# Kernel optimization log

Measured on AMD Instinct MI355X. Metric: run time of the kernel, lower is better.

Reference implementation:

```python
import jax, jax.numpy as jnp
import numpy as np

EPS = 1e-5
N = 2097152


def _bn(x, gamma, beta):
    # training-mode BatchNorm1d: biased batch stats over the batch dim
    mean = jnp.mean(x, axis=0)
    var = jnp.var(x, axis=0)
    return (x - mean) * jax.lax.rsqrt(var + EPS) * gamma + beta


def _block(x, W1, g, b, W2, b2):
    # Linear(no bias) -> BN -> ReLU -> Linear(bias)
    h = jax.nn.relu(_bn(x @ W1, g, b))
    return h @ W2 + b2


def setup_inputs() -> dict:
    key = jax.random.key(0)
    ks = jax.random.split(key, 32)
    i = iter(range(32))
    rn = lambda shape, s=0.1: (jax.random.normal(ks[next(i)], shape, dtype=jnp.float32) * s)
    d = {
        "rotation": jax.random.normal(ks[next(i)], (N, 9), dtype=jnp.float32),
        "transition": jax.random.normal(ks[next(i)], (N, 3), dtype=jnp.float32),
        # key net: 3->32 (no bias), BN32, 32->64
        "kW1": rn((3, 32)), "kg": jnp.ones(32), "kb": jnp.zeros(32),
        "kW2": rn((32, 64)), "kb2": rn((64,)),
        # query net: 9->32 (no bias), BN32, 32->64
        "qW1": rn((9, 32)), "qg": jnp.ones(32), "qb": jnp.zeros(32),
        "qW2": rn((32, 64)), "qb2": rn((64,)),
        # value net: 3->32 (no bias), BN32, 32->64
        "vW1": rn((3, 32)), "vg": jnp.ones(32), "vb": jnp.zeros(32),
        "vW2": rn((32, 64)), "vb2": rn((64,)),
        # decoder: 64->32(nb), BN32, ReLU, 32->16(nb), BN16, ReLU, 16->1(b), sigmoid
        "dW1": rn((64, 32)), "dg1": jnp.ones(32), "db1": jnp.zeros(32),
        "dW2": rn((32, 16)), "dg2": jnp.ones(16), "db2": jnp.zeros(16),
        "dW3": rn((16, 1)), "db3": rn((1,)),
    }
    return d


def reference(rotation, transition,
              kW1, kg, kb, kW2, kb2,
              qW1, qg, qb, qW2, qb2,
              vW1, vg, vb, vW2, vb2,
              dW1, dg1, db1, dW2, dg2, db2, dW3, db3):
    k = _block(transition, kW1, kg, kb, kW2, kb2)   # [N, 64]
    q = _block(rotation, qW1, qg, qb, qW2, qb2)     # [N, 64]
    v = _block(transition, vW1, vg, vb, vW2, vb2)   # [N, 64]
    attn = jax.nn.softmax(k * q, axis=-1) * v        # [N, 64]
    h = jax.nn.relu(_bn(attn @ dW1, dg1, db1))       # [N, 32]
    h = jax.nn.relu(_bn(h @ dW2, dg2, db2))          # [N, 16]
    out = jax.nn.sigmoid(h @ dW3 + db3)              # [N, 1]
    return out
```

## Files before the change

kernel.cpp:

```cpp
#include <hip/hip_runtime.h>

#define EPS 1e-5f
#define L2E 1.442695041f

typedef __attribute__((ext_vector_type(8))) short short8;
typedef __attribute__((ext_vector_type(4))) float f32x4;
#define MFMA16(a,b,c) __builtin_amdgcn_mfma_f32_16x16x32_bf16(a,b,c,0,0,0)

typedef float __attribute__((may_alias)) fal;
typedef unsigned short __attribute__((may_alias)) sal;
typedef unsigned int __attribute__((may_alias)) u32al;
typedef uint4 __attribute__((may_alias)) u4al;
typedef f32x4 __attribute__((may_alias)) f4al;

union U8 { short8 s; uint4 u; };

__device__ __forceinline__ float wred(float v){
#pragma unroll
  for(int m=32;m>=1;m>>=1) v += __shfl_xor(v,m,64);
  return v;
}

__device__ __forceinline__ unsigned short f2bf(float f){
  union{unsigned int i; float x;}v; v.x=f;
  unsigned int u=v.i;
  unsigned int r=(u + 0x7fffu + ((u>>16)&1u))>>16;
  return (unsigned short)r;
}
__device__ __forceinline__ unsigned cvtpk(float lo, float hi){
  unsigned r; asm("v_cvt_pk_bf16_f32 %0, %1, %2" : "=v"(r) : "v"(lo), "v"(hi)); return r;
}
__device__ __forceinline__ float bflo(unsigned int u){
  union{unsigned int i; float x;}v; v.i=u<<16; return v.x;
}
__device__ __forceinline__ float bfhi(unsigned int u){
  union{unsigned int i; float x;}v; v.i=u&0xffff0000u; return v.x;
}

__device__ __host__ __forceinline__ int kperm(int k){
  int g=k>>3, e=k&7;
  return (e<4) ? 4*g+e : 16+4*g+(e-4);
}
__device__ __host__ __forceinline__ int kpermD(int kg){
  int kc=kg>>5, kk=kg&31, gm=kk>>3, e=kk&7;
  return 16*(2*kc+(e>>2)) + 4*gm + (e&3);
}

__global__ __launch_bounds__(256) void kT(const float* __restrict__ kW2, const float* __restrict__ qW2,
                                          const float* __restrict__ vW2, const float* __restrict__ dW1,
                                          const float* __restrict__ dW2,
                                          unsigned short* __restrict__ wbf){
  for(int idx=threadIdx.x; idx<2048; idx+=256){
    int k=idx&31, c=idx>>5;
    int f=kperm(k);
    wbf[c*32+k]       = f2bf(kW2[f*64+c]);
    wbf[2048+c*32+k]  = f2bf(qW2[f*64+c]);
    wbf[4096+c*32+k]  = f2bf(vW2[f*64+c]);
  }
  for(int idx=threadIdx.x; idx<2048; idx+=256){
    int f=idx&31, kg=idx>>5;
    wbf[6144 + f*64 + kg] = f2bf(dW1[kpermD(kg)*32 + f]);
  }
  for(int idx=threadIdx.x; idx<512; idx+=256){
    int k=idx>>4, f=idx&15;
    wbf[8192 + f*32 + k] = f2bf(dW2[idx]);
  }
}

__global__ __launch_bounds__(256) void kA(const float* __restrict__ rot, const float* __restrict__ tra,
                                          float* __restrict__ pA, int N){
  float a[63];
#pragma unroll
  for(int i=0;i<63;i++) a[i]=0.f;
  int stride = gridDim.x*blockDim.x;
  for(int row=blockIdx.x*blockDim.x+threadIdx.x; row<N; row+=stride){
    float t[3], r[9];
#pragma unroll
    for(int i=0;i<3;i++) t[i]=tra[row*3+i];
#pragma unroll
    for(int i=0;i<9;i++) r[i]=rot[row*9+i];
#pragma unroll
    for(int i=0;i<3;i++) a[i]+=t[i];
#pragma unroll
    for(int i=0;i<3;i++)
#pragma unroll
      for(int j=i;j<3;j++) a[3 + i*3 - (i*(i-1))/2 + (j-i)] += t[i]*t[j];
#pragma unroll
    for(int i=0;i<9;i++) a[9+i]+=r[i];
#pragma unroll
    for(int i=0;i<9;i++)
#pragma unroll
      for(int j=i;j<9;j++) a[18 + i*9 - (i*(i-1))/2 + (j-i)] += r[i]*r[j];
  }
#pragma unroll
  for(int i=0;i<63;i++) a[i]=wred(a[i]);
  __shared__ __align__(16) float lds[4][63];
  int wave=threadIdx.x>>6, lane=threadIdx.x&63;
  if(lane==0){
#pragma unroll
    for(int i=0;i<63;i++) lds[wave][i]=a[i];
  }
  __syncthreads();
  int t=threadIdx.x;
  if(t<63) pA[t*gridDim.x + blockIdx.x] = lds[0][t]+lds[1][t]+lds[2][t]+lds[3][t];
}

__global__ __launch_bounds__(256) void kA2(const float* __restrict__ pA, int nb,
    const float* __restrict__ kW1, const float* __restrict__ kg, const float* __restrict__ kb,
    const float* __restrict__ qW1, const float* __restrict__ qg, const float* __restrict__ qb,
    const float* __restrict__ vW1, const float* __restrict__ vg, const float* __restrict__ vb,
    float* __restrict__ cst, unsigned short* __restrict__ wA, float invN){
  __shared__ __align__(16) float tmp[63][4];
  __shared__ __align__(16) float mom[63];
  __shared__ __align__(16) float sSc[96];
  __shared__ __align__(16) float sBi[96];
  int t=threadIdx.x;
  if(t<252){
    int f=t>>2, q=t&3;
    int per=nb/4;
    float s=0.f;
    for(int i=0;i<per;i++) s+=pA[f*nb + q*per + i];
    tmp[f][q]=s;
  }
  __syncthreads();
  if(t<63) mom[t]=tmp[t][0]+tmp[t][1]+tmp[t][2]+tmp[t][3];
  __syncthreads();
  if(t<96){
    int net=t>>5, j=t&31;
    const float* W1; const float* g; const float* b; int din, sbase, mbase, obase;
    if(net==0){W1=kW1;g=kg;b=kb;din=3;sbase=0;mbase=3;obase=0;}
    else if(net==1){W1=qW1;g=qg;b=qb;din=9;sbase=9;mbase=18;obase=64;}
    else {W1=vW1;g=vg;b=vb;din=3;sbase=0;mbase=3;obase=128;}
    float mean=0.f, ex2=0.f;
    for(int i=0;i<din;i++){
      float wi=W1[i*32+j];
      mean += mom[sbase+i]*wi;
      int rowb = mbase + i*din - (i*(i-1))/2;
      for(int i2=i;i2<din;i2++){
        float w2=W1[i2*32+j];
        float m=mom[rowb + (i2-i)];
        ex2 += ((i2==i)?1.f:2.f)*wi*w2*m;
      }
    }
    mean*=invN; ex2*=invN;
    float var=ex2-mean*mean;
    float sc=g[j]*rsqrtf(var+EPS);
    float bi=b[j]-mean*sc;
    cst[obase+j]=sc; cst[obase+32+j]=bi;
    sSc[net*32+j]=sc; sBi[net*32+j]=bi;
  }
  __syncthreads();
  for(int i=threadIdx.x; i<3072; i+=256){
    int frag=i>>9, m=(i>>5)&15, k=i&31;
    int net=frag>>1, half=frag&1;
    int f = half*16+m;
    float v=0.f;
    if(net==0){
      if(k<3) v=kW1[k*32+f]*sSc[f];
      else if(k==3) v=sBi[f];
    } else if(net==1){
      if(k>=4 && k<13) v=qW1[(k-4)*32+f]*sSc[32+f];
      else if(k==3) v=sBi[32+f];
    } else {
      if(k<3) v=vW1[k*32+f]*sSc[64+f];
      else if(k==3) v=sBi[64+f];
    }
    wA[i]=f2bf(v);
  }
}

__global__ __launch_bounds__(256) void kRed(const float* __restrict__ part, int nf, int nb,
    const float* __restrict__ g, const float* __restrict__ b, float* __restrict__ cstOut, float invN){
  int f=blockIdx.x;
  float s1=0.f,s2=0.f;
  for(int i=threadIdx.x;i<nb;i+=256){ s1+=part[f*nb+i]; s2+=part[(nf+f)*nb+i]; }
  s1=wred(s1); s2=wred(s2);
  __shared__ __align__(16) float l1[4],l2[4];
  int wave=threadIdx.x>>6;
  if((threadIdx.x&63)==0){l1[wave]=s1;l2[wave]=s2;}
  __syncthreads();
  if(threadIdx.x==0){
    float a=l1[0]+l1[1]+l1[2]+l1[3];
    float c=l2[0]+l2[1]+l2[2]+l2[3];
    float mean=a*invN;
    float var=c*invN-mean*mean;
    float sc=g[f]*rsqrtf(var+EPS);
    float bi=b[f]-mean*sc;
    cstOut[f]=sc; cstOut[nf+f]=bi;
  }
}

__global__ __launch_bounds__(256) void kHeavyM(
    const float* __restrict__ rot, const float* __restrict__ tra,
    const unsigned short* __restrict__ wA, const unsigned short* __restrict__ wbf,
    const float* __restrict__ kb2, const float* __restrict__ qb2, const float* __restrict__ vb2,
    unsigned short* __restrict__ y1o, float* __restrict__ pB, int N, int nb4)
{
  __shared__ __align__(16) unsigned short sbK[2048];
  __shared__ __align__(16) unsigned short sbQ[2048];
  __shared__ __align__(16) unsigned short sbV[2048];
  __shared__ __align__(16) unsigned short sbD[2048];
  __shared__ __align__(16) unsigned short sA[3072];
  __shared__ __align__(16) sal ybuf[4][640];
  for(int i=threadIdx.x;i<2048;i+=256){
    int e=i&7;
    int rK=i>>5, clK=(i>>3)&3;
    int dK = rK*32 + ((clK^(rK&3))<<3) + e;
    sbK[dK]=wbf[i]; sbQ[dK]=wbf[2048+i]; sbV[dK]=wbf[4096+i];
    int rD=i>>6, clD=(i>>3)&7;
    int dD = rD*64 + ((clD^(rD&7))<<3) + e;
    sbD[dD]=wbf[6144+i];
  }
  for(int i=threadIdx.x;i<3072;i+=256){
    int frag=i>>9, m=(i>>5)&15, k=i&31;
    int cl=k>>3, e=k&7;
    sA[frag*512 + m*32 + ((cl^(m&3))<<3) + e] = wA[i];
  }
  int wv=threadIdx.x>>6, lane=threadIdx.x&63;
  int c=lane&15, g=lane>>4;

  f32x4 cK[4],cQ[4],cV[4];
#pragma unroll
  for(int t=0;t<4;t++){
    cK[t]=*(const f4al*)(kb2+16*t+4*g);
    cQ[t]=*(const f4al*)(qb2+16*t+4*g);
    cV[t]=*(const f4al*)(vb2+16*t+4*g);
  }

  float stS0=0.f, stS1=0.f, stQ0=0.f, stQ1=0.f;
  __syncthreads();

  sal* yw = ybuf[wv];
  int wsw = (g^(c&3))<<3;
  f32x4 z4 = {0.f,0.f,0.f,0.f};
  int tileBase = blockIdx.x*1024 + wv*16;

  float pt0,pt1,pt2, pr[9];
  {
    int r0 = tileBase + c;
    int lr = (r0 < N) ? r0 : (N-1);
    pt0=tra[lr*3+0]; pt1=tra[lr*3+1]; pt2=tra[lr*3+2];
#pragma unroll
    for(int i=0;i<9;i++) pr[i]=rot[lr*9+i];
  }

  for(int it=0; it<16; ++it, tileBase += 64){
    if(tileBase >= N) break;
    int row = tileBase + c;
    bool vrow = row < N;

    U8 xB;
    {
      unsigned a0=cvtpk(pt0,pt1), a1=cvtpk(pt2,1.f), a2=cvtpk(pr[0],pr[1]), a3=cvtpk(pr[2],pr[3]);
      unsigned b0=cvtpk(pr[4],pr[5]), b1=cvtpk(pr[6],pr[7]), b2=cvtpk(pr[8],0.f);
      unsigned w0 = (g==0)?a0:((g==1)?b0:0u);
      unsigned w1 = (g==0)?a1:((g==1)?b1:0u);
      unsigned w2 = (g==0)?a2:((g==1)?b2:0u);
      unsigned w3 = (g==0)?a3:0u;
      xB.u = make_uint4(w0,w1,w2,w3);
    }
    {
      int r2 = tileBase + 64 + c;
      int lr2 = (r2 < N) ? r2 : (N-1);
      pt0=tra[lr2*3+0]; pt1=tra[lr2*3+1]; pt2=tra[lr2*3+2];
#pragma unroll
      for(int i=0;i<9;i++) pr[i]=rot[lr2*9+i];
    }

    U8 aK,aQ,aV;
#pragma unroll
    for(int nt=0;nt<3;nt++){
      U8 A1,A2;
      A1.u = *(const u4al*)&sA[(nt*2+0)*512 + c*32 + wsw];
      A2.u = *(const u4al*)&sA[(nt*2+1)*512 + c*32 + wsw];
      f32x4 d1 = MFMA16(A1.s, xB.s, z4);
      f32x4 d2 = MFMA16(A2.s, xB.s, z4);
#pragma unroll
      for(int rg=0;rg<4;rg++){ d1[rg]=fmaxf(d1[rg],0.f); d2[rg]=fmaxf(d2[rg],0.f); }
      uint4 u = make_uint4(cvtpk(d1[0],d1[1]),cvtpk(d1[2],d1[3]),
                           cvtpk(d2[0],d2[1]),cvtpk(d2[2],d2[3]));
      if(nt==0) aK.u=u; else if(nt==1) aQ.u=u; else aV.u=u;
    }

    f32x4 s4[4], av[4];
#pragma unroll
    for(int t=0;t<4;t++){
      U8 bk, bq, bv;
      bk.u = *(const u4al*)&sbK[(t*16+c)*32 + wsw];
      bq.u = *(const u4al*)&sbQ[(t*16+c)*32 + wsw];
      bv.u = *(const u4al*)&sbV[(t*16+c)*32 + wsw];
      f32x4 ak = MFMA16(bk.s, aK.s, cK[t]);
      f32x4 aq = MFMA16(bq.s, aQ.s, cQ[t]);
      av[t]    = MFMA16(bv.s, aV.s, cV[t]);
#pragma unroll
      for(int rg=0;rg<4;rg++) s4[t][rg]=ak[rg]*aq[rg];
    }

    float mx = s4[0][0];
#pragma unroll
    for(int t=0;t<4;t++)
#pragma unroll
      for(int rg=0;rg<4;rg++) mx=fmaxf(mx,s4[t][rg]);
    mx=fmaxf(mx,__shfl_xor(mx,16,64));
    mx=fmaxf(mx,__shfl_xor(mx,32,64));
    float m2 = mx*L2E;
    float zz = 0.f;
#pragma unroll
    for(int t=0;t<4;t++)
#pragma unroll
      for(int rg=0;rg<4;rg++){
        float e = exp2f(fmaf(s4[t][rg], L2E, -m2));
        s4[t][rg]=e; zz+=e;
      }
    zz+=__shfl_xor(zz,16,64);
    zz+=__shfl_xor(zz,32,64);
    float inv = 1.f/zz;

    U8 ap0, ap1;
    {
      float p[4][4];
#pragma unroll
      for(int t=0;t<4;t++)
#pragma unroll
        for(int rg=0;rg<4;rg++) p[t][rg]=s4[t][rg]*inv*av[t][rg];
      ap0.u = make_uint4(cvtpk(p[0][0],p[0][1]),cvtpk(p[0][2],p[0][3]),
                         cvtpk(p[1][0],p[1][1]),cvtpk(p[1][2],p[1][3]));
      ap1.u = make_uint4(cvtpk(p[2][0],p[2][1]),cvtpk(p[2][2],p[2][3]),
                         cvtpk(p[3][0],p[3][1]),cvtpk(p[3][2],p[3][3]));
    }

    f32x4 acy0=z4, acy1=z4;
#pragma unroll
    for(int kc=0;kc<2;kc++){
      int dsw = ((kc*4+g)^(c&7))<<3;
      U8 b0, b1;
      b0.u = *(const u4al*)&sbD[c*64 + dsw];
      b1.u = *(const u4al*)&sbD[(16+c)*64 + dsw];
      acy0 = MFMA16((kc?ap1:ap0).s, b0.s, acy0);
      acy1 = MFMA16((kc?ap1:ap0).s, b1.s, acy1);
    }
#pragma unroll
    for(int rg=0;rg<4;rg++){
      if(tileBase + 4*g + rg >= N){ acy0[rg]=0.f; acy1[rg]=0.f; }
    }
#pragma unroll
    for(int rg=0;rg<4;rg++){
      stS0+=acy0[rg]; stQ0+=acy0[rg]*acy0[rg];
      stS1+=acy1[rg]; stQ1+=acy1[rg]*acy1[rg];
    }
#pragma unroll
    for(int rg=0;rg<4;rg++){
      int m=4*g+rg;
      unsigned pr2 = cvtpk(acy0[rg], acy1[rg]);
      yw[m*40 + c]      = (unsigned short)pr2;
      yw[m*40 + 16 + c] = (unsigned short)(pr2>>16);
    }
    {
      u4al vv = *(const u4al*)&yw[c*40 + 8*g];
      if(vrow) *(uint4*)(y1o + (size_t)row*32 + 8*g) = vv;
    }
  }
  stS0+=__shfl_xor(stS0,16,64); stS0+=__shfl_xor(stS0,32,64);
  stS1+=__shfl_xor(stS1,16,64); stS1+=__shfl_xor(stS1,32,64);
  stQ0+=__shfl_xor(stQ0,16,64); stQ0+=__shfl_xor(stQ0,32,64);
  stQ1+=__shfl_xor(stQ1,16,64); stQ1+=__shfl_xor(stQ1,32,64);
  if(g==0){
    int b4 = blockIdx.x*4 + wv;
    pB[c*nb4 + b4]      = stS0;
    pB[(16+c)*nb4 + b4] = stS1;
    pB[(32+c)*nb4 + b4] = stQ0;
    pB[(48+c)*nb4 + b4] = stQ1;
  }
}

__global__ __launch_bounds__(256) void kCM(const unsigned short* __restrict__ y1,
    const float* __restrict__ cst, const unsigned short* __restrict__ wbf,
    unsigned short* __restrict__ y2o, float* __restrict__ pC, int N, int nb){
  __shared__ __align__(16) unsigned short ybuf[4][256];
  __shared__ __align__(16) float sStat[4][32];
  int wv=threadIdx.x>>6, lane=threadIdx.x&63;
  int c=lane&15, g=lane>>4;
  U8 bD2; bD2.u = *(const uint4*)(wbf + 8192 + c*32 + 8*g);
  float sc[8], bi[8];
#pragma unroll
  for(int i=0;i<8;i++){ sc[i]=cst[192+8*g+i]; bi[i]=cst[224+8*g+i]; }
  float stS=0.f, stQ=0.f;
  unsigned short* yb = ybuf[wv];
  int tileBase = blockIdx.x*1024 + wv*16;
  f32x4 z4 = {0.f,0.f,0.f,0.f};
  uint4 w;
  {
    int r0 = tileBase + c;
    int lr = (r0 < N) ? r0 : (N-1);
    w = *(const uint4*)(y1 + (size_t)lr*32 + 8*g);
  }
  for(int it=0; it<16; ++it, tileBase += 64){
    if(tileBase >= N) break;
    int row = tileBase + c;
    bool vrow = row < N;
    uint4 cur = w;
    {
      int r2 = tileBase + 64 + c;
      int lr2 = (r2 < N) ? r2 : (N-1);
      w = *(const uint4*)(y1 + (size_t)lr2*32 + 8*g);
    }
    unsigned wu[4]={cur.x,cur.y,cur.z,cur.w};
    float h[8];
#pragma unroll
    for(int j=0;j<4;j++){ h[2*j]=bflo(wu[j]); h[2*j+1]=bfhi(wu[j]); }
#pragma unroll
    for(int i=0;i<8;i++){ float x=h[i]*sc[i]+bi[i]; h[i]=fmaxf(x,0.f); }
    U8 a;
    a.u = make_uint4(cvtpk(h[0],h[1]),cvtpk(h[2],h[3]),cvtpk(h[4],h[5]),cvtpk(h[6],h[7]));
    f32x4 acc = MFMA16(a.s, bD2.s, z4);
#pragma unroll
    for(int rg=0;rg<4;rg++){
      if(tileBase + 4*g + rg >= N) acc[rg]=0.f;
      stS+=acc[rg]; stQ+=acc[rg]*acc[rg];
    }
#pragma unroll
    for(int rg=0;rg<4;rg++){
      int m=4*g+rg;
      yb[(m*16 + c) ^ ((m&3)<<2)] = f2bf(acc[rg]);
    }
    {
      int idx = (c*16 + 4*g) ^ ((c&3)<<2);
      uint2 vv = *(uint2*)&yb[idx];
      if(vrow) *(uint2*)(y2o + (size_t)row*16 + 4*g) = vv;
    }
  }
  stS+=__shfl_xor(stS,16,64); stS+=__shfl_xor(stS,32,64);
  stQ+=__shfl_xor(stQ,16,64); stQ+=__shfl_xor(stQ,32,64);
  if(g==0){ sStat[wv][c]=stS; sStat[wv][16+c]=stQ; }
  __syncthreads();
  int t=threadIdx.x;
  if(t<32) pC[t*nb + blockIdx.x] = sStat[0][t]+sStat[1][t]+sStat[2][t]+sStat[3][t];
}

__global__ __launch_bounds__(256) void kD(const unsigned short* __restrict__ y2,
    const float* __restrict__ cst, const float* __restrict__ dW3, const float* __restrict__ db3,
    float* __restrict__ outp, int N){
  int row=blockIdx.x*256+threadIdx.x;
  if(row>=N) return;
  const uint4* src=(const uint4*)(y2+(size_t)row*16);
  uint4 q0=src[0],q1=src[1];
  unsigned int w[8]={q0.x,q0.y,q0.z,q0.w,q1.x,q1.y,q1.z,q1.w};
  float o=db3[0];
#pragma unroll
  for(int kk=0;kk<8;kk++){
    float lo=bflo(w[kk])*cst[256+2*kk]+cst[272+2*kk];
    float hi=bfhi(w[kk])*cst[256+2*kk+1]+cst[272+2*kk+1];
    lo=lo>0.f?lo:0.f; hi=hi>0.f?hi:0.f;
    o+=lo*dW3[2*kk]+hi*dW3[2*kk+1];
  }
  outp[row]=1.f/(1.f+__expf(-o));
}

extern "C" void kernel_launch(void* const* d_in, const int* in_sizes, int n_in,
                              void* d_out, int out_size, void* d_ws, size_t ws_size,
                              hipStream_t stream){
  const float* rot=(const float*)d_in[0];
  const float* tra=(const float*)d_in[1];
  const float* kW1=(const float*)d_in[2];
  const float* kg =(const float*)d_in[3];
  const float* kb =(const float*)d_in[4];
  const float* kW2=(const float*)d_in[5];
  const float* kb2=(const float*)d_in[6];
  const float* qW1=(const float*)d_in[7];
  const float* qg =(const float*)d_in[8];
  const float* qb =(const float*)d_in[9];
  const float* qW2=(const float*)d_in[10];
  const float* qb2=(const float*)d_in[11];
  const float* vW1=(const float*)d_in[12];
  const float* vg =(const float*)d_in[13];
  const float* vb =(const float*)d_in[14];
  const float* vW2=(const float*)d_in[15];
  const float* vb2=(const float*)d_in[16];
  const float* dW1=(const float*)d_in[17];
  const float* dg1=(const float*)d_in[18];
  const float* db1=(const float*)d_in[19];
  const float* dW2=(const float*)d_in[20];
  const float* dg2=(const float*)d_in[21];
  const float* db2=(const float*)d_in[22];
  const float* dW3=(const float*)d_in[23];
  const float* db3=(const float*)d_in[24];

  int N=in_sizes[0]/9;
  int nbH=(N+1023)/1024;
  int nb4=4*nbH;

  float* ws=(float*)d_ws;
  float* cst=ws;
  float* pA =ws+1024;
  float* pB =ws+33280;
  float* pC =pB+(size_t)64*nb4;
  unsigned short* wbf=(unsigned short*)(pC+(size_t)32*nbH);
  unsigned short* wA = wbf+8704;

  size_t y1off=(size_t)8<<20;
  unsigned short* y1=(unsigned short*)((char*)d_ws + y1off);
  unsigned short* y2=(unsigned short*)((char*)d_ws + y1off + (size_t)N*64);
  float invN=1.f/(float)N;
  dim3 B(256);

  kT <<<dim3(1),   B,0,stream>>>(kW2,qW2,vW2,dW1,dW2,wbf);
  kA <<<dim3(512), B,0,stream>>>(rot,tra,pA,N);
  kA2<<<dim3(1),   B,0,stream>>>(pA,512,kW1,kg,kb,qW1,qg,qb,vW1,vg,vb,cst,wA,invN);

  kHeavyM<<<dim3(nbH),B,0,stream>>>(rot,tra,wA,wbf,kb2,qb2,vb2,y1,pB,N,nb4);
  kRed<<<dim3(32),B,0,stream>>>(pB,32,nb4,dg1,db1,cst+192,invN);
  kCM<<<dim3(nbH),B,0,stream>>>(y1,cst,wbf,y2,pC,N,nbH);
  kRed<<<dim3(16),B,0,stream>>>(pC,16,nbH,dg2,db2,cst+256,invN);
  kD <<<dim3((N+255)/256),B,0,stream>>>(y2,cst,dW3,db3,(float*)d_out,N);
}
```

Baseline: 246.5 us.

## Vectorize stats loads, move bias to LDS, tree-reduce softmax max/sum

The first-stage statistics kernel now handles four rows per thread and loads them with float4 vector loads instead of scalar strided loads. A single thread of block 0 processes any tail rows. In the heavy kernel, the per-thread bias registers are replaced by LDS reads at each MFMA, which lowers register pressure at the cost of extra LDS traffic. The softmax max and sum reductions are rewritten as balanced trees to shorten the serial dependency chains.

```diff
diff --git a/kernel.cpp b/kernel.cpp
--- a/kernel.cpp
+++ b/kernel.cpp
@@ -73,24 +73,52 @@
 #pragma unroll
   for(int i=0;i<63;i++) a[i]=0.f;
   int stride = gridDim.x*blockDim.x;
-  for(int row=blockIdx.x*blockDim.x+threadIdx.x; row<N; row+=stride){
-    float t[3], r[9];
-#pragma unroll
-    for(int i=0;i<3;i++) t[i]=tra[row*3+i];
-#pragma unroll
-    for(int i=0;i<9;i++) r[i]=rot[row*9+i];
-#pragma unroll
-    for(int i=0;i<3;i++) a[i]+=t[i];
-#pragma unroll
-    for(int i=0;i<3;i++)
-#pragma unroll
-      for(int j=i;j<3;j++) a[3 + i*3 - (i*(i-1))/2 + (j-i)] += t[i]*t[j];
-#pragma unroll
-    for(int i=0;i<9;i++) a[9+i]+=r[i];
-#pragma unroll
-    for(int i=0;i<9;i++)
-#pragma unroll
-      for(int j=i;j<9;j++) a[18 + i*9 - (i*(i-1))/2 + (j-i)] += r[i]*r[j];
+  int nch = N>>2;
+  for(int ch=blockIdx.x*blockDim.x+threadIdx.x; ch<nch; ch+=stride){
+    float tt[12], rr[36];
+    {
+      const float4* tp = (const float4*)(tra + (size_t)ch*12);
+      const float4* rp = (const float4*)(rot + (size_t)ch*36);
+#pragma unroll
+      for(int i=0;i<3;i++) *(float4*)&tt[4*i]=tp[i];
+#pragma unroll
+      for(int i=0;i<9;i++) *(float4*)&rr[4*i]=rp[i];
+    }
+#pragma unroll
+    for(int w=0;w<4;w++){
+      const float* t=&tt[3*w];
+      const float* r=&rr[9*w];
+#pragma unroll
+      for(int i=0;i<3;i++) a[i]+=t[i];
+#pragma unroll
+      for(int i=0;i<3;i++)
+#pragma unroll
+        for(int j=i;j<3;j++) a[3 + i*3 - (i*(i-1))/2 + (j-i)] += t[i]*t[j];
+#pragma unroll
+      for(int i=0;i<9;i++) a[9+i]+=r[i];
+#pragma unroll
+      for(int i=0;i<9;i++)
+#pragma unroll
+        for(int j=i;j<9;j++) a[18 + i*9 - (i*(i-1))/2 + (j-i)] += r[i]*r[j];
+    }
+  }
+  if(blockIdx.x==0 && threadIdx.x==0){
+    for(int row=(nch<<2); row<N; ++row){
+      const float* t=tra+ (size_t)row*3;
+      const float* r=rot+ (size_t)row*9;
+#pragma unroll
+      for(int i=0;i<3;i++) a[i]+=t[i];
+#pragma unroll
+      for(int i=0;i<3;i++)
+#pragma unroll
+        for(int j=i;j<3;j++) a[3 + i*3 - (i*(i-1))/2 + (j-i)] += t[i]*t[j];
+#pragma unroll
+      for(int i=0;i<9;i++) a[9+i]+=r[i];
+#pragma unroll
+      for(int i=0;i<9;i++)
+#pragma unroll
+        for(int j=i;j<9;j++) a[18 + i*9 - (i*(i-1))/2 + (j-i)] += r[i]*r[j];
+    }
   }
 #pragma unroll
   for(int i=0;i<63;i++) a[i]=wred(a[i]);
@@ -196,12 +224,17 @@
     const float* __restrict__ kb2, const float* __restrict__ qb2, const float* __restrict__ vb2,
     unsigned short* __restrict__ y1o, float* __restrict__ pB, int N, int nb4)
 {
+  __shared__ __align__(16) float sBias[192];
   __shared__ __align__(16) unsigned short sbK[2048];
   __shared__ __align__(16) unsigned short sbQ[2048];
   __shared__ __align__(16) unsigned short sbV[2048];
   __shared__ __align__(16) unsigned short sbD[2048];
   __shared__ __align__(16) unsigned short sA[3072];
   __shared__ __align__(16) sal ybuf[4][640];
+  if(threadIdx.x<192){
+    int i=threadIdx.x;
+    sBias[i] = (i<64)?kb2[i]:((i<128)?qb2[i-64]:vb2[i-128]);
+  }
   for(int i=threadIdx.x;i<2048;i+=256){
     int e=i&7;
     int rK=i>>5, clK=(i>>3)&3;
@@ -219,14 +252,6 @@
   int wv=threadIdx.x>>6, lane=threadIdx.x&63;
   int c=lane&15, g=lane>>4;
 
-  f32x4 cK[4],cQ[4],cV[4];
-#pragma unroll
-  for(int t=0;t<4;t++){
-    cK[t]=*(const f4al*)(kb2+16*t+4*g);
-    cQ[t]=*(const f4al*)(qb2+16*t+4*g);
-    cV[t]=*(const f4al*)(vb2+16*t+4*g);
-  }
-
   float stS0=0.f, stS1=0.f, stQ0=0.f, stQ1=0.f;
   __syncthreads();
 
@@ -289,29 +314,37 @@
       bk.u = *(const u4al*)&sbK[(t*16+c)*32 + wsw];
       bq.u = *(const u4al*)&sbQ[(t*16+c)*32 + wsw];
       bv.u = *(const u4al*)&sbV[(t*16+c)*32 + wsw];
-      f32x4 ak = MFMA16(bk.s, aK.s, cK[t]);
-      f32x4 aq = MFMA16(bq.s, aQ.s, cQ[t]);
-      av[t]    = MFMA16(bv.s, aV.s, cV[t]);
+      f32x4 ak = MFMA16(bk.s, aK.s, *(const f4al*)&sBias[16*t+4*g]);
+      f32x4 aq = MFMA16(bq.s, aQ.s, *(const f4al*)&sBias[64+16*t+4*g]);
+      av[t]    = MFMA16(bv.s, aV.s, *(const f4al*)&sBias[128+16*t+4*g]);
 #pragma unroll
       for(int rg=0;rg<4;rg++) s4[t][rg]=ak[rg]*aq[rg];
     }
 
-    float mx = s4[0][0];
-#pragma unroll
-    for(int t=0;t<4;t++)
-#pragma unroll
-      for(int rg=0;rg<4;rg++) mx=fmaxf(mx,s4[t][rg]);
+    float m0,m1,m2_,m3,m4,m5,m6,m7;
+    m0=fmaxf(s4[0][0],s4[0][1]); m1=fmaxf(s4[0][2],s4[0][3]);
+    m2_=fmaxf(s4[1][0],s4[1][1]); m3=fmaxf(s4[1][2],s4[1][3]);
+    m4=fmaxf(s4[2][0],s4[2][1]); m5=fmaxf(s4[2][2],s4[2][3]);
+    m6=fmaxf(s4[3][0],s4[3][1]); m7=fmaxf(s4[3][2],s4[3][3]);
+    m0=fmaxf(m0,m1); m2_=fmaxf(m2_,m3); m4=fmaxf(m4,m5); m6=fmaxf(m6,m7);
+    m0=fmaxf(m0,m2_); m4=fmaxf(m4,m6);
+    float mx=fmaxf(m0,m4);
     mx=fmaxf(mx,__shfl_xor(mx,16,64));
     mx=fmaxf(mx,__shfl_xor(mx,32,64));
     float m2 = mx*L2E;
-    float zz = 0.f;
+    float ee[16];
 #pragma unroll
     for(int t=0;t<4;t++)
 #pragma unroll
       for(int rg=0;rg<4;rg++){
         float e = exp2f(fmaf(s4[t][rg], L2E, -m2));
-        s4[t][rg]=e; zz+=e;
+        s4[t][rg]=e; ee[t*4+rg]=e;
       }
+#pragma unroll
+    for(int i=0;i<8;i++) ee[i]+=ee[i+8];
+#pragma unroll
+    for(int i=0;i<4;i++) ee[i]+=ee[i+4];
+    float zz=(ee[0]+ee[1])+(ee[2]+ee[3]);
     zz+=__shfl_xor(zz,16,64);
     zz+=__shfl_xor(zz,32,64);
     float inv = 1.f/zz;
```

New measurement: 237.3 us. 3.7% less time.
